# Kernel optimization log

Measured on AMD Instinct MI355X. Metric: run time of the kernel, lower is better.

## Reference

```python
import jax, jax.numpy as jnp
import numpy as np

B, S, D, E = 4, 4096, 1024, 8
TOP_K = 2


def setup_inputs() -> dict:
    key = jax.random.key(0)
    k_x, k_gw, k_gb, k_ew, k_eb = jax.random.split(key, 5)
    x = jax.random.normal(k_x, (B, S, D), dtype=jnp.float32)
    gate_w = jax.random.normal(k_gw, (E, D), dtype=jnp.float32) * 0.02
    gate_b = jax.random.normal(k_gb, (E,), dtype=jnp.float32) * 0.02
    expert_w = jax.random.normal(k_ew, (E, D, D), dtype=jnp.float32) * 0.02
    expert_b = jax.random.normal(k_eb, (E, D), dtype=jnp.float32) * 0.02
    return {"x": x, "gate_w": gate_w, "gate_b": gate_b,
            "expert_w": expert_w, "expert_b": expert_b}


def reference(x, gate_w, gate_b, expert_w, expert_b):
    b, s, d = x.shape
    h = x.reshape(-1, d)                                  # [T, D]
    # router: linear -> softmax (fp32) -> top-k -> renormalize
    router_logits = h @ gate_w.T + gate_b                 # [T, E]
    probs = jax.nn.softmax(router_logits.astype(jnp.float32), axis=-1)
    topw, sel = jax.lax.top_k(probs, TOP_K)               # [T, K]
    topw = topw / jnp.sum(topw, axis=-1, keepdims=True)
    topw = topw.astype(h.dtype)
    out = jnp.zeros_like(h)
    for e in range(E):  # small fixed loop over experts
        # per-token combine weight for expert e (0 if not selected)
        we = jnp.sum(jnp.where(sel == e, topw, 0.0), axis=-1)  # [T]
        out = out + (h @ expert_w[e].T + expert_b[e]) * we[:, None]
    return out.reshape(b, s, d), router_logits
```

## Files before the change

### kernel.cpp

```cpp
#include <hip/hip_runtime.h>
#include <hip/hip_bf16.h>

typedef unsigned short u16;
typedef unsigned int u32;

#define T_TOK 16384
#define DIM   1024
#define NEXP  8

#define XB_OFF      0
#define WB_OFF      33554432
#define CNT_OFF     50331648
#define LIST_OFF    50332160
#define SELW_OFF    50856448
#define CONTRIB_OFF 51380736
#define WS_NEED     118489600ULL

__device__ __forceinline__ u16 f2bf(float f) {
    u32 u = __float_as_uint(f);
    u += 0x7fff + ((u >> 16) & 1);
    return (u16)(u >> 16);
}
__device__ __forceinline__ float bf2f(u16 u) {
    return __uint_as_float(((u32)u) << 16);
}

__global__ __launch_bounds__(128) void k_zero(int* counts) {
    if (threadIdx.x < NEXP * 16) counts[threadIdx.x] = 0;
}

__global__ __launch_bounds__(256) void k_cvt(const float* __restrict__ in,
                                             u16* __restrict__ out, int n4) {
    int i = blockIdx.x * 256 + threadIdx.x;
    if (i >= n4) return;
    float4 v = reinterpret_cast<const float4*>(in)[i];
    ushort4 u;
    u.x = f2bf(v.x); u.y = f2bf(v.y); u.z = f2bf(v.z); u.w = f2bf(v.w);
    reinterpret_cast<ushort4*>(out)[i] = u;
}

#define RT_PB 32

__global__ __launch_bounds__(256) void k_router(
    const float* __restrict__ x, const float* __restrict__ gw,
    const float* __restrict__ gb, float* __restrict__ logits,
    u16* __restrict__ xb, int* __restrict__ counts,
    int* __restrict__ lists, float4* __restrict__ selw)
{
    const int tid  = threadIdx.x;
    const int lane = tid & 63;
    const int w    = tid >> 6;

    __shared__ int   s_sel0[RT_PB], s_sel1[RT_PB];
    __shared__ int   s_lcnt[NEXP], s_gbase[NEXP];

    if (tid < NEXP) s_lcnt[tid] = 0;

    for (int i = 0; i < 8; ++i) {
        const int l = w * 8 + i;
        const int t = blockIdx.x * RT_PB + l;

        const float* xr = x + (size_t)t * DIM;
        float4 xs[4];
#pragma unroll
        for (int j = 0; j < 4; ++j)
            xs[j] = *reinterpret_cast<const float4*>(xr + (j * 64 + lane) * 4);

        float acc[NEXP];
#pragma unroll
        for (int e = 0; e < NEXP; ++e) {
            const float* gr = gw + e * DIM;
            float s = 0.f;
#pragma unroll
            for (int j = 0; j < 4; ++j) {
                float4 g = *reinterpret_cast<const float4*>(gr + (j * 64 + lane) * 4);
                s += xs[j].x * g.x + xs[j].y * g.y + xs[j].z * g.z + xs[j].w * g.w;
            }
            acc[e] = s;
        }
#pragma unroll
        for (int off = 1; off < 64; off <<= 1) {
#pragma unroll
            for (int e = 0; e < NEXP; ++e) acc[e] += __shfl_xor(acc[e], off);
        }
#pragma unroll
        for (int e = 0; e < NEXP; ++e) acc[e] += gb[e];

        int i0 = 0; float v0 = acc[0];
#pragma unroll
        for (int e = 1; e < NEXP; ++e) if (acc[e] > v0) { v0 = acc[e]; i0 = e; }
        int i1 = -1; float v1 = -3.4e38f;
#pragma unroll
        for (int e = 0; e < NEXP; ++e) if (e != i0 && acc[e] > v1) { v1 = acc[e]; i1 = e; }
        float e1  = __expf(v1 - v0);
        float inv = 1.f / (1.f + e1);
        float w0 = inv, w1 = e1 * inv;

        u16* xrow = xb + (size_t)t * DIM;
#pragma unroll
        for (int j = 0; j < 4; ++j) {
            int c = (j * 64 + lane) * 4;
            float4 v = xs[j];
            ushort4 u;
            u.x = f2bf(v.x); u.y = f2bf(v.y); u.z = f2bf(v.z); u.w = f2bf(v.w);
            *reinterpret_cast<ushort4*>(xrow + c) = u;
        }
        if (lane == 0) {
            float4 lo = make_float4(acc[0], acc[1], acc[2], acc[3]);
            float4 hi = make_float4(acc[4], acc[5], acc[6], acc[7]);
            *reinterpret_cast<float4*>(logits + (size_t)t * NEXP)     = lo;
            *reinterpret_cast<float4*>(logits + (size_t)t * NEXP + 4) = hi;
            selw[t] = make_float4(__int_as_float(i0), __int_as_float(i1), w0, w1);
            s_sel0[l] = i0; s_sel1[l] = i1;
        }
    }
    __syncthreads();

    int i0 = 0, i1 = 0, r0 = 0, r1 = 0;
    if (tid < RT_PB) {
        i0 = s_sel0[tid]; i1 = s_sel1[tid];
        r0 = atomicAdd(&s_lcnt[i0], 1);
        r1 = atomicAdd(&s_lcnt[i1], 1);
    }
    __syncthreads();
    if (tid < NEXP)
        s_gbase[tid] = atomicAdd(&counts[tid * 16], s_lcnt[tid]);
    __syncthreads();
    if (tid < RT_PB) {
        int t  = blockIdx.x * RT_PB + tid;
        lists[i0 * T_TOK + s_gbase[i0] + r0] = t * 2;
        lists[i1 * T_TOK + s_gbase[i1] + r1] = t * 2 + 1;
    }
}


typedef __attribute__((ext_vector_type(8))) short bf16x8;
typedef __attribute__((ext_vector_type(4))) float f32x4;

#define GLDS16(g, l) __builtin_amdgcn_global_load_lds( \
    (const __attribute__((address_space(1))) void*)(g), \
    (__attribute__((address_space(3))) void*)(l), 16, 0, 0)

#define BAR() __builtin_amdgcn_s_barrier()
#define PRIO1() __builtin_amdgcn_s_setprio(1)
#define PRIO0() __builtin_amdgcn_s_setprio(0)
#define VMW4() asm volatile("s_waitcnt vmcnt(4)" ::: "memory")
#define VMW0() asm volatile("s_waitcnt vmcnt(0)" ::: "memory")

template<int ATOMIC>
__global__ __launch_bounds__(512, 2) void k_gemm(
    const u16* __restrict__ xb, const u16* __restrict__ wb,
    const int* __restrict__ counts, const int* __restrict__ lists,
    const float4* __restrict__ selw, u16* __restrict__ contrib,
    float* __restrict__ out)
{
    __shared__ u16 lds[65536];

    const int bid = (blockIdx.x & 7) * 256 + (blockIdx.x >> 3);
    const int e   = bid >> 8;
    const int nt  = (bid >> 6) & 3;
    const int mt  = bid & 63;
    const int cnt = counts[e * 16];
    if (mt * 256 >= cnt) return;

    const int tid  = threadIdx.x;
    const int lane = tid & 63;
    const int wid  = tid >> 6;
    const int wm   = wid >> 2;
    const int wn   = wid & 3;
    const int listbase = e * T_TOK;

    const int srow = tid >> 2;
    const int cA   = (((tid & 3) - (tid >> 3)) & 3) * 8;
    int tokA[2];
#pragma unroll
    for (int l = 0; l < 2; ++l) {
        int slot = mt * 256 + l * 128 + srow;
        tokA[l] = lists[listbase + (slot < cnt ? slot : cnt - 1)] >> 1;
    }
    const u16* srcA0 = xb + (size_t)tokA[0] * DIM + cA;
    const u16* srcA1 = xb + (size_t)tokA[1] * DIM + cA;
    const u16* srcB0 = wb + ((size_t)e << 20) + (size_t)(nt * 256 + srow) * DIM + cA;
    const u16* srcB1 = srcB0 + (size_t)128 * DIM;

#define STAGE_A(nb, ks, kk) do { \
    GLDS16(srcA0 + (kk) + (ks) * 32, &lds[(nb) * 32768 + (ks) * 8192 + wid * 512]); \
    GLDS16(srcA1 + (kk) + (ks) * 32, &lds[(nb) * 32768 + (ks) * 8192 + 4096 + wid * 512]); } while (0)
#define STAGE_B(nb, ks, kk) do { \
    GLDS16(srcB0 + (kk) + (ks) * 32, &lds[(nb) * 32768 + 16384 + (ks) * 8192 + wid * 512]); \
    GLDS16(srcB1 + (kk) + (ks) * 32, &lds[(nb) * 32768 + 16384 + (ks) * 8192 + 4096 + wid * 512]); } while (0)

    const int cs8  = ((((lane >> 4) + ((lane >> 1) & 3)) & 3)) * 8;
    const int offA = (wm * 128 + (lane & 15)) * 32 + cs8;
    const int offB = 16384 + (wn * 64 + (lane & 15)) * 32 + cs8;

    bf16x8 Af[4], Bf[4];
    f32x4 acc[8][4];
#pragma unroll
    for (int mi = 0; mi < 8; ++mi)
#pragma unroll
        for (int ni = 0; ni < 4; ++ni) acc[mi][ni] = (f32x4)0.f;

#define LDA4(buf, ks, q) do { \
    Af[0] = *(const bf16x8*)&lds[(buf) * 32768 + (ks) * 8192 + ((q) * 4 + 0) * 512 + offA]; \
    Af[1] = *(const bf16x8*)&lds[(buf) * 32768 + (ks) * 8192 + ((q) * 4 + 1) * 512 + offA]; \
    Af[2] = *(const bf16x8*)&lds[(buf) * 32768 + (ks) * 8192 + ((q) * 4 + 2) * 512 + offA]; \
    Af[3] = *(const bf16x8*)&lds[(buf) * 32768 + (ks) * 8192 + ((q) * 4 + 3) * 512 + offA]; } while (0)
#define LDB4(buf, ks) do { \
    Bf[0] = *(const bf16x8*)&lds[(buf) * 32768 + (ks) * 8192 + 0 * 512 + offB]; \
    Bf[1] = *(const bf16x8*)&lds[(buf) * 32768 + (ks) * 8192 + 1 * 512 + offB]; \
    Bf[2] = *(const bf16x8*)&lds[(buf) * 32768 + (ks) * 8192 + 2 * 512 + offB]; \
    Bf[3] = *(const bf16x8*)&lds[(buf) * 32768 + (ks) * 8192 + 3 * 512 + offB]; } while (0)
#define MFMA_ROW(q, i) do { \
    acc[(q)*4+(i)][0] = __builtin_amdgcn_mfma_f32_16x16x32_bf16(Af[i], Bf[0], acc[(q)*4+(i)][0], 0, 0, 0); \
    acc[(q)*4+(i)][1] = __builtin_amdgcn_mfma_f32_16x16x32_bf16(Af[i], Bf[1], acc[(q)*4+(i)][1], 0, 0, 0); \
    acc[(q)*4+(i)][2] = __builtin_amdgcn_mfma_f32_16x16x32_bf16(Af[i], Bf[2], acc[(q)*4+(i)][2], 0, 0, 0); \
    acc[(q)*4+(i)][3] = __builtin_amdgcn_mfma_f32_16x16x32_bf16(Af[i], Bf[3], acc[(q)*4+(i)][3], 0, 0, 0); } while (0)
#define MFMA16(q) do { MFMA_ROW(q, 0); MFMA_ROW(q, 1); MFMA_ROW(q, 2); MFMA_ROW(q, 3); } while (0)

    STAGE_A(0, 0, 0); STAGE_B(0, 0, 0); STAGE_A(0, 1, 0); STAGE_B(0, 1, 0);
    VMW0();
    BAR();

    for (int t = 0; t < 15; ++t) {
        const int buf = t & 1, nb = buf ^ 1;
        const int kn  = (t + 1) * 64;
        STAGE_A(nb, 0, kn);
        LDB4(buf, 0); LDA4(buf, 0, 0);
        BAR(); PRIO1(); MFMA16(0); PRIO0(); BAR();
        STAGE_B(nb, 0, kn);
        LDA4(buf, 0, 1);
        BAR(); PRIO1(); MFMA16(1); PRIO0();
        VMW4(); BAR();
        STAGE_A(nb, 1, kn);
        LDB4(buf, 1); LDA4(buf, 1, 0);
        BAR(); PRIO1(); MFMA16(0); PRIO0(); BAR();
        STAGE_B(nb, 1, kn);
        LDA4(buf, 1, 1);
        BAR(); PRIO1(); MFMA16(1); PRIO0();
        VMW4(); BAR();
    }
    {
        LDB4(1, 0); LDA4(1, 0, 0);
        BAR(); PRIO1(); MFMA16(0); PRIO0(); BAR();
        LDA4(1, 0, 1);
        BAR(); PRIO1(); MFMA16(1); PRIO0();
        VMW0(); BAR();
        LDB4(1, 1); LDA4(1, 1, 0);
        BAR(); PRIO1(); MFMA16(0); PRIO0(); BAR();
        LDA4(1, 1, 1);
        BAR(); PRIO1(); MFMA16(1); PRIO0();
    }

    const int rbase = (lane >> 4) * 4;
    const int cbase = nt * 256 + wn * 64 + (lane & 15);
#pragma unroll
    for (int mi = 0; mi < 8; ++mi) {
#pragma unroll
        for (int r = 0; r < 4; ++r) {
            int slot = mt * 256 + wm * 128 + mi * 16 + rbase + r;
            if (slot < cnt) {
                int lv = lists[listbase + slot];
                if (ATOMIC) {
                    int tok = lv >> 1;
                    float4 sw = selw[tok];
                    float wgt = (lv & 1) ? sw.w : sw.z;
                    float* orow = out + (size_t)tok * DIM + cbase;
#pragma unroll
                    for (int ni = 0; ni < 4; ++ni)
                        atomicAdd(orow + ni * 16, acc[mi][ni][r] * wgt);
                } else {
                    u16* crow = contrib + (size_t)lv * DIM + cbase;
#pragma unroll
                    for (int ni = 0; ni < 4; ++ni)
                        crow[ni * 16] = f2bf(acc[mi][ni][r]);
                }
            }
        }
    }
}

__global__ __launch_bounds__(256) void k_combine(
    const u16* __restrict__ contrib, const float4* __restrict__ selw,
    const float* __restrict__ eb, float* __restrict__ out)
{
    const int lane = threadIdx.x & 63;
    const int t    = blockIdx.x * 4 + (threadIdx.x >> 6);
    float4 sw = selw[t];
    const int e0 = __float_as_int(sw.x);
    const int e1 = __float_as_int(sw.y);
    const float w0 = sw.z, w1 = sw.w;
    const u16* c0 = contrib + (size_t)(t * 2) * DIM;
    const u16* c1 = c0 + DIM;
    const float* b0 = eb + e0 * DIM;
    const float* b1 = eb + e1 * DIM;
    float* orow = out + (size_t)t * DIM;
#pragma unroll
    for (int j = 0; j < 2; ++j) {
        const int c = (j * 64 + lane) * 8;
        uint4 u0 = *reinterpret_cast<const uint4*>(c0 + c);
        uint4 u1 = *reinterpret_cast<const uint4*>(c1 + c);
        const u16* p0 = (const u16*)&u0;
        const u16* p1 = (const u16*)&u1;
        float4 r0, r1;
#pragma unroll
        for (int h = 0; h < 2; ++h) {
            float4 bb0 = *reinterpret_cast<const float4*>(b0 + c + h * 4);
            float4 bb1 = *reinterpret_cast<const float4*>(b1 + c + h * 4);
            float4 o;
            o.x = w0 * (bf2f(p0[h*4+0]) + bb0.x) + w1 * (bf2f(p1[h*4+0]) + bb1.x);
            o.y = w0 * (bf2f(p0[h*4+1]) + bb0.y) + w1 * (bf2f(p1[h*4+1]) + bb1.y);
            o.z = w0 * (bf2f(p0[h*4+2]) + bb0.z) + w1 * (bf2f(p1[h*4+2]) + bb1.z);
            o.w = w0 * (bf2f(p0[h*4+3]) + bb0.w) + w1 * (bf2f(p1[h*4+3]) + bb1.w);
            *reinterpret_cast<float4*>(orow + c + h * 4) = o;
        }
        (void)r0; (void)r1;
    }
}

__global__ __launch_bounds__(256) void k_bias(
    const float4* __restrict__ selw, const float* __restrict__ eb,
    float* __restrict__ out)
{
    const int lane = threadIdx.x & 63;
    const int t    = blockIdx.x * 4 + (threadIdx.x >> 6);
    float4 sw = selw[t];
    const float* b0 = eb + __float_as_int(sw.x) * DIM;
    const float* b1 = eb + __float_as_int(sw.y) * DIM;
    float* orow = out + (size_t)t * DIM;
#pragma unroll
    for (int j = 0; j < 4; ++j) {
        int c = (j * 64 + lane) * 4;
        float4 f0 = *reinterpret_cast<const float4*>(b0 + c);
        float4 f1 = *reinterpret_cast<const float4*>(b1 + c);
        float4 o;
        o.x = sw.z * f0.x + sw.w * f1.x;
        o.y = sw.z * f0.y + sw.w * f1.y;
        o.z = sw.z * f0.z + sw.w * f1.z;
        o.w = sw.z * f0.w + sw.w * f1.w;
        *reinterpret_cast<float4*>(orow + c) = o;
    }
}

extern "C" void kernel_launch(void* const* d_in, const int* in_sizes, int n_in,
                              void* d_out, int out_size, void* d_ws, size_t ws_size,
                              hipStream_t stream) {
    const float* x  = (const float*)d_in[0];
    const float* gw = (const float*)d_in[1];
    const float* gb = (const float*)d_in[2];
    const float* ew = (const float*)d_in[3];
    const float* eb = (const float*)d_in[4];

    float* out    = (float*)d_out;
    float* logits = out + (size_t)T_TOK * DIM;

    char*   ws      = (char*)d_ws;
    u16*    xb      = (u16*)(ws + XB_OFF);
    u16*    wb      = (u16*)(ws + WB_OFF);
    int*    counts  = (int*)(ws + CNT_OFF);
    int*    lists   = (int*)(ws + LIST_OFF);
    float4* selw    = (float4*)(ws + SELW_OFF);
    u16*    contrib = (u16*)(ws + CONTRIB_OFF);

    k_zero<<<1, 128, 0, stream>>>(counts);
    k_cvt<<<(NEXP * DIM * DIM / 4 + 255) / 256, 256, 0, stream>>>(ew, wb, NEXP * DIM * DIM / 4);
    k_router<<<T_TOK / RT_PB, 256, 0, stream>>>(x, gw, gb, logits, xb, counts, lists, selw);

    if (ws_size >= WS_NEED) {
        k_gemm<0><<<NEXP * 64 * 4, 512, 0, stream>>>(xb, wb, counts, lists, selw, contrib, out);
        k_combine<<<T_TOK / 4, 256, 0, stream>>>(contrib, selw, eb, out);
    } else {
        k_bias<<<T_TOK / 4, 256, 0, stream>>>(selw, eb, out);
        k_gemm<1><<<NEXP * 64 * 4, 512, 0, stream>>>(xb, wb, counts, lists, selw, contrib, out);
    }
}
```

Measured before the change: 175.9 us.

## Shrink expert GEMM tiles to 128x128 and fuse weight conversion into router

Replaces the 256x256-tile, 512-thread expert GEMM with a 128x128-tile, 256-thread version that uses half the LDS, a simpler single-stage pipeline per k-half and a plain block index mapping (expert, m-tile, n-tile). The expert weight fp32->bf16 conversion moves from its own kernel into a grid-stride loop at the end of the router kernel, which removes one launch. Smaller tiles should give more blocks and better load balance across uneven per-expert counts, but they lower operand reuse and drop the XCD-aware block swizzle. The initial wait now uses vmcnt(4) after staging eight loads, so the first tile may be read before its loads have finished (a correctness risk).

```diff
diff --git a/kernel.cpp b/kernel.cpp
--- a/kernel.cpp
+++ b/kernel.cpp
@@ -29,23 +29,14 @@
     if (threadIdx.x < NEXP * 16) counts[threadIdx.x] = 0;
 }
 
-__global__ __launch_bounds__(256) void k_cvt(const float* __restrict__ in,
-                                             u16* __restrict__ out, int n4) {
-    int i = blockIdx.x * 256 + threadIdx.x;
-    if (i >= n4) return;
-    float4 v = reinterpret_cast<const float4*>(in)[i];
-    ushort4 u;
-    u.x = f2bf(v.x); u.y = f2bf(v.y); u.z = f2bf(v.z); u.w = f2bf(v.w);
-    reinterpret_cast<ushort4*>(out)[i] = u;
-}
-
 #define RT_PB 32
 
 __global__ __launch_bounds__(256) void k_router(
     const float* __restrict__ x, const float* __restrict__ gw,
     const float* __restrict__ gb, float* __restrict__ logits,
     u16* __restrict__ xb, int* __restrict__ counts,
-    int* __restrict__ lists, float4* __restrict__ selw)
+    int* __restrict__ lists, float4* __restrict__ selw,
+    const float* __restrict__ ew, u16* __restrict__ wb)
 {
     const int tid  = threadIdx.x;
     const int lane = tid & 63;
@@ -131,6 +122,15 @@
         lists[i0 * T_TOK + s_gbase[i0] + r0] = t * 2;
         lists[i1 * T_TOK + s_gbase[i1] + r1] = t * 2 + 1;
     }
+
+    const int n4 = NEXP * DIM * DIM / 4;
+    const int stride = gridDim.x * 256;
+    for (int i = blockIdx.x * 256 + tid; i < n4; i += stride) {
+        float4 v = reinterpret_cast<const float4*>(ew)[i];
+        ushort4 u;
+        u.x = f2bf(v.x); u.y = f2bf(v.y); u.z = f2bf(v.z); u.w = f2bf(v.w);
+        reinterpret_cast<ushort4*>(wb)[i] = u;
+    }
 }
 
 
@@ -148,26 +148,26 @@
 #define VMW0() asm volatile("s_waitcnt vmcnt(0)" ::: "memory")
 
 template<int ATOMIC>
-__global__ __launch_bounds__(512, 2) void k_gemm(
+__global__ __launch_bounds__(256, 2) void k_gemm(
     const u16* __restrict__ xb, const u16* __restrict__ wb,
     const int* __restrict__ counts, const int* __restrict__ lists,
     const float4* __restrict__ selw, u16* __restrict__ contrib,
     float* __restrict__ out)
 {
-    __shared__ u16 lds[65536];
-
-    const int bid = (blockIdx.x & 7) * 256 + (blockIdx.x >> 3);
-    const int e   = bid >> 8;
-    const int nt  = (bid >> 6) & 3;
-    const int mt  = bid & 63;
+    __shared__ u16 lds[32768];
+
+    const int bid = blockIdx.x;
+    const int e   = bid >> 10;
+    const int mt  = (bid >> 3) & 127;
+    const int nt  = bid & 7;
     const int cnt = counts[e * 16];
-    if (mt * 256 >= cnt) return;
+    if (mt * 128 >= cnt) return;
 
     const int tid  = threadIdx.x;
     const int lane = tid & 63;
     const int wid  = tid >> 6;
-    const int wm   = wid >> 2;
-    const int wn   = wid & 3;
+    const int wm   = wid >> 1;
+    const int wn   = wid & 1;
     const int listbase = e * T_TOK;
 
     const int srow = tid >> 2;
@@ -175,90 +175,78 @@
     int tokA[2];
 #pragma unroll
     for (int l = 0; l < 2; ++l) {
-        int slot = mt * 256 + l * 128 + srow;
+        int slot = mt * 128 + l * 64 + srow;
         tokA[l] = lists[listbase + (slot < cnt ? slot : cnt - 1)] >> 1;
     }
     const u16* srcA0 = xb + (size_t)tokA[0] * DIM + cA;
     const u16* srcA1 = xb + (size_t)tokA[1] * DIM + cA;
-    const u16* srcB0 = wb + ((size_t)e << 20) + (size_t)(nt * 256 + srow) * DIM + cA;
-    const u16* srcB1 = srcB0 + (size_t)128 * DIM;
-
-#define STAGE_A(nb, ks, kk) do { \
-    GLDS16(srcA0 + (kk) + (ks) * 32, &lds[(nb) * 32768 + (ks) * 8192 + wid * 512]); \
-    GLDS16(srcA1 + (kk) + (ks) * 32, &lds[(nb) * 32768 + (ks) * 8192 + 4096 + wid * 512]); } while (0)
-#define STAGE_B(nb, ks, kk) do { \
-    GLDS16(srcB0 + (kk) + (ks) * 32, &lds[(nb) * 32768 + 16384 + (ks) * 8192 + wid * 512]); \
-    GLDS16(srcB1 + (kk) + (ks) * 32, &lds[(nb) * 32768 + 16384 + (ks) * 8192 + 4096 + wid * 512]); } while (0)
-
-    const int cs8  = ((((lane >> 4) + ((lane >> 1) & 3)) & 3)) * 8;
-    const int offA = (wm * 128 + (lane & 15)) * 32 + cs8;
-    const int offB = 16384 + (wn * 64 + (lane & 15)) * 32 + cs8;
+    const u16* srcB0 = wb + ((size_t)e << 20) + (size_t)(nt * 128 + srow) * DIM + cA;
+    const u16* srcB1 = srcB0 + (size_t)64 * DIM;
+
+#define STAGE(nb, ks, kk) do { \
+    GLDS16(srcA0 + (kk) + (ks) * 32, &lds[(nb) * 16384 + (ks) * 4096 + wid * 512]); \
+    GLDS16(srcA1 + (kk) + (ks) * 32, &lds[(nb) * 16384 + (ks) * 4096 + 2048 + wid * 512]); \
+    GLDS16(srcB0 + (kk) + (ks) * 32, &lds[(nb) * 16384 + 8192 + (ks) * 4096 + wid * 512]); \
+    GLDS16(srcB1 + (kk) + (ks) * 32, &lds[(nb) * 16384 + 8192 + (ks) * 4096 + 2048 + wid * 512]); } while (0)
+
+    const int cs8  = (((lane >> 4) + ((lane >> 1) & 3)) & 3) * 8;
+    const int offA = (wm * 64 + (lane & 15)) * 32 + cs8;
+    const int offB = 8192 + (wn * 64 + (lane & 15)) * 32 + cs8;
 
     bf16x8 Af[4], Bf[4];
-    f32x4 acc[8][4];
-#pragma unroll
-    for (int mi = 0; mi < 8; ++mi)
+    f32x4 acc[4][4];
+#pragma unroll
+    for (int mi = 0; mi < 4; ++mi)
 #pragma unroll
         for (int ni = 0; ni < 4; ++ni) acc[mi][ni] = (f32x4)0.f;
 
-#define LDA4(buf, ks, q) do { \
-    Af[0] = *(const bf16x8*)&lds[(buf) * 32768 + (ks) * 8192 + ((q) * 4 + 0) * 512 + offA]; \
-    Af[1] = *(const bf16x8*)&lds[(buf) * 32768 + (ks) * 8192 + ((q) * 4 + 1) * 512 + offA]; \
-    Af[2] = *(const bf16x8*)&lds[(buf) * 32768 + (ks) * 8192 + ((q) * 4 + 2) * 512 + offA]; \
-    Af[3] = *(const bf16x8*)&lds[(buf) * 32768 + (ks) * 8192 + ((q) * 4 + 3) * 512 + offA]; } while (0)
+#define LDA4(buf, ks) do { \
+    Af[0] = *(const bf16x8*)&lds[(buf) * 16384 + (ks) * 4096 + 0 * 512 + offA]; \
+    Af[1] = *(const bf16x8*)&lds[(buf) * 16384 + (ks) * 4096 + 1 * 512 + offA]; \
+    Af[2] = *(const bf16x8*)&lds[(buf) * 16384 + (ks) * 4096 + 2 * 512 + offA]; \
+    Af[3] = *(const bf16x8*)&lds[(buf) * 16384 + (ks) * 4096 + 3 * 512 + offA]; } while (0)
 #define LDB4(buf, ks) do { \
-    Bf[0] = *(const bf16x8*)&lds[(buf) * 32768 + (ks) * 8192 + 0 * 512 + offB]; \
-    Bf[1] = *(const bf16x8*)&lds[(buf) * 32768 + (ks) * 8192 + 1 * 512 + offB]; \
-    Bf[2] = *(const bf16x8*)&lds[(buf) * 32768 + (ks) * 8192 + 2 * 512 + offB]; \
-    Bf[3] = *(const bf16x8*)&lds[(buf) * 32768 + (ks) * 8192 + 3 * 512 + offB]; } while (0)
-#define MFMA_ROW(q, i) do { \
-    acc[(q)*4+(i)][0] = __builtin_amdgcn_mfma_f32_16x16x32_bf16(Af[i], Bf[0], acc[(q)*4+(i)][0], 0, 0, 0); \
-    acc[(q)*4+(i)][1] = __builtin_amdgcn_mfma_f32_16x16x32_bf16(Af[i], Bf[1], acc[(q)*4+(i)][1], 0, 0, 0); \
-    acc[(q)*4+(i)][2] = __builtin_amdgcn_mfma_f32_16x16x32_bf16(Af[i], Bf[2], acc[(q)*4+(i)][2], 0, 0, 0); \
-    acc[(q)*4+(i)][3] = __builtin_amdgcn_mfma_f32_16x16x32_bf16(Af[i], Bf[3], acc[(q)*4+(i)][3], 0, 0, 0); } while (0)
-#define MFMA16(q) do { MFMA_ROW(q, 0); MFMA_ROW(q, 1); MFMA_ROW(q, 2); MFMA_ROW(q, 3); } while (0)
-
-    STAGE_A(0, 0, 0); STAGE_B(0, 0, 0); STAGE_A(0, 1, 0); STAGE_B(0, 1, 0);
-    VMW0();
-    BAR();
+    Bf[0] = *(const bf16x8*)&lds[(buf) * 16384 + (ks) * 4096 + 0 * 512 + offB]; \
+    Bf[1] = *(const bf16x8*)&lds[(buf) * 16384 + (ks) * 4096 + 1 * 512 + offB]; \
+    Bf[2] = *(const bf16x8*)&lds[(buf) * 16384 + (ks) * 4096 + 2 * 512 + offB]; \
+    Bf[3] = *(const bf16x8*)&lds[(buf) * 16384 + (ks) * 4096 + 3 * 512 + offB]; } while (0)
+#define MFMA_ROW(i) do { \
+    acc[i][0] = __builtin_amdgcn_mfma_f32_16x16x32_bf16(Af[i], Bf[0], acc[i][0], 0, 0, 0); \
+    acc[i][1] = __builtin_amdgcn_mfma_f32_16x16x32_bf16(Af[i], Bf[1], acc[i][1], 0, 0, 0); \
+    acc[i][2] = __builtin_amdgcn_mfma_f32_16x16x32_bf16(Af[i], Bf[2], acc[i][2], 0, 0, 0); \
+    acc[i][3] = __builtin_amdgcn_mfma_f32_16x16x32_bf16(Af[i], Bf[3], acc[i][3], 0, 0, 0); } while (0)
+#define MFMA16() do { MFMA_ROW(0); MFMA_ROW(1); MFMA_ROW(2); MFMA_ROW(3); } while (0)
+
+    STAGE(0, 0, 0); STAGE(0, 1, 0);
+    VMW4(); BAR();
 
     for (int t = 0; t < 15; ++t) {
         const int buf = t & 1, nb = buf ^ 1;
         const int kn  = (t + 1) * 64;
-        STAGE_A(nb, 0, kn);
-        LDB4(buf, 0); LDA4(buf, 0, 0);
-        BAR(); PRIO1(); MFMA16(0); PRIO0(); BAR();
-        STAGE_B(nb, 0, kn);
-        LDA4(buf, 0, 1);
-        BAR(); PRIO1(); MFMA16(1); PRIO0();
+        STAGE(nb, 0, kn);
+        LDA4(buf, 0); LDB4(buf, 0);
+        PRIO1(); MFMA16(); PRIO0();
         VMW4(); BAR();
-        STAGE_A(nb, 1, kn);
-        LDB4(buf, 1); LDA4(buf, 1, 0);
-        BAR(); PRIO1(); MFMA16(0); PRIO0(); BAR();
-        STAGE_B(nb, 1, kn);
-        LDA4(buf, 1, 1);
-        BAR(); PRIO1(); MFMA16(1); PRIO0();
+        STAGE(nb, 1, kn);
+        LDA4(buf, 1); LDB4(buf, 1);
+        PRIO1(); MFMA16(); PRIO0();
         VMW4(); BAR();
     }
     {
-        LDB4(1, 0); LDA4(1, 0, 0);
-        BAR(); PRIO1(); MFMA16(0); PRIO0(); BAR();
-        LDA4(1, 0, 1);
-        BAR(); PRIO1(); MFMA16(1); PRIO0();
+        LDA4(1, 0); LDB4(1, 0);
+        PRIO1(); MFMA16(); PRIO0();
         VMW0(); BAR();
-        LDB4(1, 1); LDA4(1, 1, 0);
-        BAR(); PRIO1(); MFMA16(0); PRIO0(); BAR();
-        LDA4(1, 1, 1);
-        BAR(); PRIO1(); MFMA16(1); PRIO0();
+        LDA4(1, 1); LDB4(1, 1);
+        PRIO1(); MFMA16(); PRIO0();
     }
 
     const int rbase = (lane >> 4) * 4;
-    const int cbase = nt * 256 + wn * 64 + (lane & 15);
-#pragma unroll
-    for (int mi = 0; mi < 8; ++mi) {
+    const int cbase = nt * 128 + wn * 64 + (lane & 15);
+#pragma unroll
+    for (int mi = 0; mi < 4; ++mi) {
 #pragma unroll
         for (int r = 0; r < 4; ++r) {
-            int slot = mt * 256 + wm * 128 + mi * 16 + rbase + r;
+            int slot = mt * 128 + wm * 64 + mi * 16 + rbase + r;
             if (slot < cnt) {
                 int lv = lists[listbase + slot];
                 if (ATOMIC) {
@@ -302,7 +290,6 @@
         uint4 u1 = *reinterpret_cast<const uint4*>(c1 + c);
         const u16* p0 = (const u16*)&u0;
         const u16* p1 = (const u16*)&u1;
-        float4 r0, r1;
 #pragma unroll
         for (int h = 0; h < 2; ++h) {
             float4 bb0 = *reinterpret_cast<const float4*>(b0 + c + h * 4);
@@ -314,7 +301,6 @@
             o.w = w0 * (bf2f(p0[h*4+3]) + bb0.w) + w1 * (bf2f(p1[h*4+3]) + bb1.w);
             *reinterpret_cast<float4*>(orow + c + h * 4) = o;
         }
-        (void)r0; (void)r1;
     }
 }
 
@@ -363,14 +349,15 @@
     u16*    contrib = (u16*)(ws + CONTRIB_OFF);
 
     k_zero<<<1, 128, 0, stream>>>(counts);
-    k_cvt<<<(NEXP * DIM * DIM / 4 + 255) / 256, 256, 0, stream>>>(ew, wb, NEXP * DIM * DIM / 4);
-    k_router<<<T_TOK / RT_PB, 256, 0, stream>>>(x, gw, gb, logits, xb, counts, lists, selw);
-
+    k_router<<<T_TOK / RT_PB, 256, 0, stream>>>(x, gw, gb, logits, xb, counts,
+                                                lists, selw, ew, wb);
+
+    const int grid = NEXP * 128 * 8;
     if (ws_size >= WS_NEED) {
-        k_gemm<0><<<NEXP * 64 * 4, 512, 0, stream>>>(xb, wb, counts, lists, selw, contrib, out);
+        k_gemm<0><<<grid, 256, 0, stream>>>(xb, wb, counts, lists, selw, contrib, out);
         k_combine<<<T_TOK / 4, 256, 0, stream>>>(contrib, selw, eb, out);
     } else {
         k_bias<<<T_TOK / 4, 256, 0, stream>>>(selw, eb, out);
-        k_gemm<1><<<NEXP * 64 * 4, 512, 0, stream>>>(xb, wb, counts, lists, selw, contrib, out);
-    }
-}
+        k_gemm<1><<<grid, 256, 0, stream>>>(xb, wb, counts, lists, selw, contrib, out);
+    }
+}
```

Measured after the change: 177.3 us. No clear change (+0.8%).
